# Performance work log

Hardware: AMD Instinct MI355X
Metric: run time of the kernel (lower is better)

Reference implementation:

```python
import jax, jax.numpy as jnp
import numpy as np

OBS_LEN = 16          # observation_len in SnapKV
KERNEL = 5            # AvgPool1d kernel_size
MAX_CACHE_LEN = 2048  # max_cache_length


def _avg_pool1d_nopad(x, k=KERNEL):
    """AvgPool1d(kernel=k, stride=1, padding=k//2, count_include_pad=False) over last axis."""
    S = x.shape[-1]
    pad = k // 2
    zero = jnp.zeros(x.shape[:-1] + (1,), x.dtype)
    c0 = jnp.concatenate([zero, jnp.cumsum(x, axis=-1)], axis=-1)  # [..., S+1]
    i = jnp.arange(S)
    hi = jnp.minimum(i + pad + 1, S)  # exclusive window end
    lo = jnp.maximum(i - pad, 0)      # inclusive window start
    wsum = jnp.take(c0, hi, axis=-1) - jnp.take(c0, lo, axis=-1)
    return wsum / (hi - lo).astype(x.dtype)


def setup_inputs() -> dict:
    key = jax.random.key(0)
    k1, k2, k3 = jax.random.split(key, 3)
    B, H, Q, S, D = 1, 32, 64, 8192, 128
    # realistic attention weights: softmax over key axis
    attn = jax.nn.softmax(jax.random.normal(k1, (B, H, Q, S), jnp.float32), axis=-1)
    k_val = jax.random.normal(k2, (B, H, S, D), jnp.float32)
    v_val = jax.random.normal(k3, (B, H, S, D), jnp.float32)
    input_pos = jnp.arange(S, dtype=jnp.int32)
    return {"attn": attn, "k_val": k_val, "v_val": v_val, "input_pos": input_pos}


def reference(attn, k_val, v_val, input_pos):
    # ---- SnapKV prompt compression (_compress_prompt_w_snapkv) ----
    # priority: mean attention received by each key over the last OBS_LEN queries
    priority = attn[:, :, -OBS_LEN:, :].mean(axis=2)          # [B, H, S]
    attn_history = priority                                    # pre-pooling copy
    pooled = _avg_pool1d_nopad(priority)                       # [B, H, S]
    pooled = pooled.at[:, :, -OBS_LEN:].set(1.0)               # always keep observation window
    _, keep_idxs = jax.lax.top_k(pooled, MAX_CACHE_LEN)        # [B, H, L]
    keep_idxs = jnp.sort(keep_idxs, axis=-1)
    attn_history_c = jnp.take_along_axis(attn_history, keep_idxs, axis=-1)  # [B, H, L]
    idx4 = keep_idxs[..., None]                                # [B, H, L, 1]
    k_compressed = jnp.take_along_axis(k_val, idx4, axis=2)    # [B, H, L, D]
    v_compressed = jnp.take_along_axis(v_val, idx4, axis=2)    # [B, H, L, D]
    # ---- cache fill (update / fill_headwise): compressed tokens fill the whole cache ----
    k_cache = k_compressed
    v_cache = v_compressed
    pos = keep_idxs[0].astype(jnp.int32)                       # head-specific positions, [H, L]
    return k_cache, v_cache, attn_history_c, pos
```

## Files before the change

### kernel.cpp

```cpp
#include <hip/hip_runtime.h>

#define H 32
#define Q 64
#define S 8192
#define D 128
#define OBS 16
#define L 2048

__global__ void k_priority(const float* __restrict__ attn, float* __restrict__ prio) {
    int gid = blockIdx.x;
    int h = gid >> 3;
    int chunk = gid & 7;
    int s4 = chunk * 1024 + threadIdx.x * 4;
    const float4* base = (const float4*)(attn + ((size_t)(h * Q + (Q - OBS)) * S + s4));
    float4 acc = make_float4(0.f, 0.f, 0.f, 0.f);
#pragma unroll
    for (int qq = 0; qq < OBS; ++qq) {
        float4 v = base[qq * (S / 4)];
        acc.x += v.x; acc.y += v.y; acc.z += v.z; acc.w += v.w;
    }
    const float inv = 1.0f / (float)OBS;
    acc.x *= inv; acc.y *= inv; acc.z *= inv; acc.w *= inv;
    *((float4*)(prio + (size_t)h * S + s4)) = acc;
}

__global__ __launch_bounds__(1024) void k_select(const float* __restrict__ prio,
                                                 int* __restrict__ keep,
                                                 float* __restrict__ hist_out,
                                                 float* __restrict__ pos_out) {
    __shared__ float pr[S];
    __shared__ int scan_buf[1024];
    __shared__ unsigned red[16];
    const int h = blockIdx.x;
    const int tid = threadIdx.x;
    const int lane = tid & 63, wid = tid >> 6;

    {
        const float4* src = (const float4*)(prio + (size_t)h * S);
        float4* dst4 = (float4*)pr;
        for (int i = tid; i < S / 4; i += 1024) dst4[i] = src[i];
    }
    __syncthreads();

    unsigned key[8];
    const int s0 = tid * 8;
#pragma unroll
    for (int j = 0; j < 8; ++j) {
        int s = s0 + j;
        float pooled;
        if (s >= S - OBS) {
            pooled = 1.0f;
        } else {
            int lo = s - 2; if (lo < 0) lo = 0;
            int hi = s + 3; if (hi > S) hi = S;
            float sum = 0.f;
            for (int i = lo; i < hi; ++i) sum += pr[i];
            pooled = sum / (float)(hi - lo);
        }
        key[j] = __float_as_uint(pooled);
    }

    unsigned prefix = 0;
    int k = L;
    for (int b = 31; b >= 0; --b) {
        const unsigned bit = 1u << b;
        const unsigned want = prefix | bit;
        const unsigned mask = ~(bit - 1u);
        int cnt = 0;
#pragma unroll
        for (int j = 0; j < 8; ++j) cnt += ((key[j] & mask) == want) ? 1 : 0;
        unsigned c = (unsigned)cnt;
        for (int off = 32; off > 0; off >>= 1) c += __shfl_down(c, off);
        if (lane == 0) red[wid] = c;
        __syncthreads();
        unsigned total = 0;
#pragma unroll
        for (int w = 0; w < 16; ++w) total += red[w];
        __syncthreads();
        if ((int)total >= k) prefix = want; else k -= (int)total;
    }
    const unsigned T = prefix;
    const int needed_eq = k;

    int local_eq = 0;
#pragma unroll
    for (int j = 0; j < 8; ++j) local_eq += (key[j] == T) ? 1 : 0;
    scan_buf[tid] = local_eq;
    __syncthreads();
    for (int off = 1; off < 1024; off <<= 1) {
        int v = scan_buf[tid];
        int add = (tid >= off) ? scan_buf[tid - off] : 0;
        __syncthreads();
        scan_buf[tid] = v + add;
        __syncthreads();
    }
    const int eq_before = scan_buf[tid] - local_eq;

    int sel_mask = 0, sel_count = 0;
    {
        int eqrank = eq_before;
#pragma unroll
        for (int j = 0; j < 8; ++j) {
            bool gt = key[j] > T;
            bool eq = key[j] == T;
            bool sl = gt || (eq && (eqrank < needed_eq));
            if (eq) eqrank++;
            if (sl) { sel_mask |= (1 << j); sel_count++; }
        }
    }
    __syncthreads();

    scan_buf[tid] = sel_count;
    __syncthreads();
    for (int off = 1; off < 1024; off <<= 1) {
        int v = scan_buf[tid];
        int add = (tid >= off) ? scan_buf[tid - off] : 0;
        __syncthreads();
        scan_buf[tid] = v + add;
        __syncthreads();
    }
    int r = scan_buf[tid] - sel_count;

#pragma unroll
    for (int j = 0; j < 8; ++j) {
        if (sel_mask & (1 << j)) {
            int s = s0 + j;
            size_t o = (size_t)h * L + r;
            keep[o] = s;
            pos_out[o] = (float)s;
            hist_out[o] = pr[s];
            r++;
        }
    }
}

__global__ void k_gather(const float* __restrict__ kvK, const float* __restrict__ kvV,
                         const int* __restrict__ keep, float* __restrict__ out) {
    const int tid = threadIdx.x;
    const int row = blockIdx.x * 8 + (tid >> 5);
    const int lane = tid & 31;
    const int tensor = row >> 16;
    const int idx = row & 65535;
    const int h = idx >> 11;
    const int s = keep[idx];
    const float* srcbase = tensor ? kvV : kvK;
    const float4* src = (const float4*)(srcbase + (size_t)(h * S + s) * D);
    float4* dst = (float4*)(out + (size_t)tensor * ((size_t)H * L * D) + (size_t)idx * D);
    dst[lane] = src[lane];
}

extern "C" void kernel_launch(void* const* d_in, const int* in_sizes, int n_in,
                              void* d_out, int out_size, void* d_ws, size_t ws_size,
                              hipStream_t stream) {
    const float* attn = (const float*)d_in[0];
    const float* k_val = (const float*)d_in[1];
    const float* v_val = (const float*)d_in[2];

    float* out = (float*)d_out;
    float* hist = out + (size_t)2 * H * L * D;
    float* pos = hist + (size_t)H * L;

    float* prio = (float*)d_ws;
    int* keep = (int*)((char*)d_ws + (size_t)H * S * sizeof(float));

    k_priority<<<256, 256, 0, stream>>>(attn, prio);
    k_select<<<H, 1024, 0, stream>>>(prio, keep, hist, pos);
    k_gather<<<(2 * H * L) / 8, 256, 0, stream>>>(k_val, v_val, keep, out);
}
```

Measured before the change: 310.0 us.

## Fuse priority reduction into select and replace block scans with wave scans

Folds the observation-window mean into the per-head select kernel, which removes one launch and the priority round-trip through global memory. The pooling window is now loaded into registers once rather than re-read from shared memory, and the radix-select reduction uses shared atomics, cutting one barrier per bit. The two block-wide Hillis-Steele scans become one wave-level shuffle scan on packed greater/equal counts, so ranks are computed directly. The gather handles K and V in the same thread, which halves the block count. The trade-off is that the attention read now runs on only 32 blocks, which may underuse bandwidth compared with the 256-block priority kernel.

```diff
diff --git a/kernel.cpp b/kernel.cpp
--- a/kernel.cpp
+++ b/kernel.cpp
@@ -7,57 +7,63 @@
 #define OBS 16
 #define L 2048
 
-__global__ void k_priority(const float* __restrict__ attn, float* __restrict__ prio) {
-    int gid = blockIdx.x;
-    int h = gid >> 3;
-    int chunk = gid & 7;
-    int s4 = chunk * 1024 + threadIdx.x * 4;
-    const float4* base = (const float4*)(attn + ((size_t)(h * Q + (Q - OBS)) * S + s4));
-    float4 acc = make_float4(0.f, 0.f, 0.f, 0.f);
-#pragma unroll
-    for (int qq = 0; qq < OBS; ++qq) {
-        float4 v = base[qq * (S / 4)];
-        acc.x += v.x; acc.y += v.y; acc.z += v.z; acc.w += v.w;
-    }
-    const float inv = 1.0f / (float)OBS;
-    acc.x *= inv; acc.y *= inv; acc.z *= inv; acc.w *= inv;
-    *((float4*)(prio + (size_t)h * S + s4)) = acc;
-}
-
-__global__ __launch_bounds__(1024) void k_select(const float* __restrict__ prio,
+__global__ __launch_bounds__(1024) void k_select(const float* __restrict__ attn,
                                                  int* __restrict__ keep,
                                                  float* __restrict__ hist_out,
                                                  float* __restrict__ pos_out) {
     __shared__ float pr[S];
-    __shared__ int scan_buf[1024];
-    __shared__ unsigned red[16];
+    __shared__ int wtot[16];
+    __shared__ int rcount[32];
     const int h = blockIdx.x;
     const int tid = threadIdx.x;
     const int lane = tid & 63, wid = tid >> 6;
 
+    if (tid < 32) rcount[tid] = 0;
+
     {
-        const float4* src = (const float4*)(prio + (size_t)h * S);
-        float4* dst4 = (float4*)pr;
-        for (int i = tid; i < S / 4; i += 1024) dst4[i] = src[i];
+        const float* abase = attn + ((size_t)(h * Q + (Q - OBS))) * S;
+        float4 a0 = make_float4(0.f, 0.f, 0.f, 0.f);
+        float4 a1 = make_float4(0.f, 0.f, 0.f, 0.f);
+#pragma unroll
+        for (int q = 0; q < OBS; ++q) {
+            const float4* row = (const float4*)(abase + (size_t)q * S);
+            float4 v0 = row[tid];
+            float4 v1 = row[tid + 1024];
+            a0.x += v0.x; a0.y += v0.y; a0.z += v0.z; a0.w += v0.w;
+            a1.x += v1.x; a1.y += v1.y; a1.z += v1.z; a1.w += v1.w;
+        }
+        const float inv = 1.0f / (float)OBS;
+        a0.x *= inv; a0.y *= inv; a0.z *= inv; a0.w *= inv;
+        a1.x *= inv; a1.y *= inv; a1.z *= inv; a1.w *= inv;
+        ((float4*)pr)[tid] = a0;
+        ((float4*)pr)[tid + 1024] = a1;
     }
     __syncthreads();
 
     unsigned key[8];
     const int s0 = tid * 8;
+    {
+        float w[12];
 #pragma unroll
-    for (int j = 0; j < 8; ++j) {
-        int s = s0 + j;
-        float pooled;
-        if (s >= S - OBS) {
-            pooled = 1.0f;
-        } else {
-            int lo = s - 2; if (lo < 0) lo = 0;
-            int hi = s + 3; if (hi > S) hi = S;
-            float sum = 0.f;
-            for (int i = lo; i < hi; ++i) sum += pr[i];
-            pooled = sum / (float)(hi - lo);
+        for (int i = 0; i < 12; ++i) {
+            int idx = s0 - 2 + i;
+            w[i] = (idx >= 0 && idx < S) ? pr[idx] : 0.f;
         }
-        key[j] = __float_as_uint(pooled);
+#pragma unroll
+        for (int j = 0; j < 8; ++j) {
+            int s = s0 + j;
+            float pooled;
+            if (s >= S - OBS) {
+                pooled = 1.0f;
+            } else {
+                int lo = s - 2; if (lo < 0) lo = 0;
+                int hi = s + 3;
+                float sum = 0.f;
+                for (int i = lo; i < hi; ++i) sum += w[i - s0 + 2];
+                pooled = sum / (float)(hi - lo);
+            }
+            key[j] = __float_as_uint(pooled);
+        }
     }
 
     unsigned prefix = 0;
@@ -69,84 +75,71 @@
         int cnt = 0;
 #pragma unroll
         for (int j = 0; j < 8; ++j) cnt += ((key[j] & mask) == want) ? 1 : 0;
-        unsigned c = (unsigned)cnt;
-        for (int off = 32; off > 0; off >>= 1) c += __shfl_down(c, off);
-        if (lane == 0) red[wid] = c;
+#pragma unroll
+        for (int off = 32; off > 0; off >>= 1) cnt += __shfl_down(cnt, off);
+        if (lane == 0) atomicAdd(&rcount[b], cnt);
         __syncthreads();
-        unsigned total = 0;
-#pragma unroll
-        for (int w = 0; w < 16; ++w) total += red[w];
-        __syncthreads();
-        if ((int)total >= k) prefix = want; else k -= (int)total;
+        int total = rcount[b];
+        if (total >= k) prefix = want; else k -= total;
     }
     const unsigned T = prefix;
     const int needed_eq = k;
 
-    int local_eq = 0;
+    int gt = 0, eq = 0;
 #pragma unroll
-    for (int j = 0; j < 8; ++j) local_eq += (key[j] == T) ? 1 : 0;
-    scan_buf[tid] = local_eq;
+    for (int j = 0; j < 8; ++j) {
+        gt += (key[j] > T) ? 1 : 0;
+        eq += (key[j] == T) ? 1 : 0;
+    }
+    int packed = (gt << 16) | eq;
+    int v = packed;
+#pragma unroll
+    for (int off = 1; off < 64; off <<= 1) {
+        int u = __shfl_up(v, off);
+        if (lane >= off) v += u;
+    }
+    if (lane == 63) wtot[wid] = v;
     __syncthreads();
-    for (int off = 1; off < 1024; off <<= 1) {
-        int v = scan_buf[tid];
-        int add = (tid >= off) ? scan_buf[tid - off] : 0;
-        __syncthreads();
-        scan_buf[tid] = v + add;
-        __syncthreads();
-    }
-    const int eq_before = scan_buf[tid] - local_eq;
+    int base = 0;
+    for (int w = 0; w < wid; ++w) base += wtot[w];
+    int excl = base + v - packed;
+    int gt_before = excl >> 16;
+    int eq_before = excl & 0xffff;
 
-    int sel_mask = 0, sel_count = 0;
     {
-        int eqrank = eq_before;
+        int g = gt_before, e = eq_before;
 #pragma unroll
         for (int j = 0; j < 8; ++j) {
-            bool gt = key[j] > T;
-            bool eq = key[j] == T;
-            bool sl = gt || (eq && (eqrank < needed_eq));
-            if (eq) eqrank++;
-            if (sl) { sel_mask |= (1 << j); sel_count++; }
-        }
-    }
-    __syncthreads();
-
-    scan_buf[tid] = sel_count;
-    __syncthreads();
-    for (int off = 1; off < 1024; off <<= 1) {
-        int v = scan_buf[tid];
-        int add = (tid >= off) ? scan_buf[tid - off] : 0;
-        __syncthreads();
-        scan_buf[tid] = v + add;
-        __syncthreads();
-    }
-    int r = scan_buf[tid] - sel_count;
-
-#pragma unroll
-    for (int j = 0; j < 8; ++j) {
-        if (sel_mask & (1 << j)) {
-            int s = s0 + j;
-            size_t o = (size_t)h * L + r;
-            keep[o] = s;
-            pos_out[o] = (float)s;
-            hist_out[o] = pr[s];
-            r++;
+            bool isgt = key[j] > T;
+            bool iseq = key[j] == T;
+            bool sel = isgt || (iseq && (e < needed_eq));
+            if (sel) {
+                int s = s0 + j;
+                int rank = g + (e < needed_eq ? e : needed_eq);
+                size_t o = (size_t)h * L + rank;
+                keep[o] = s;
+                pos_out[o] = (float)s;
+                hist_out[o] = pr[s];
+            }
+            g += isgt ? 1 : 0;
+            e += iseq ? 1 : 0;
         }
     }
 }
 
-__global__ void k_gather(const float* __restrict__ kvK, const float* __restrict__ kvV,
+__global__ void k_gather(const float* __restrict__ kv_k, const float* __restrict__ kv_v,
                          const int* __restrict__ keep, float* __restrict__ out) {
     const int tid = threadIdx.x;
-    const int row = blockIdx.x * 8 + (tid >> 5);
+    const int idx = blockIdx.x * 8 + (tid >> 5);
     const int lane = tid & 31;
-    const int tensor = row >> 16;
-    const int idx = row & 65535;
     const int h = idx >> 11;
     const int s = keep[idx];
-    const float* srcbase = tensor ? kvV : kvK;
-    const float4* src = (const float4*)(srcbase + (size_t)(h * S + s) * D);
-    float4* dst = (float4*)(out + (size_t)tensor * ((size_t)H * L * D) + (size_t)idx * D);
-    dst[lane] = src[lane];
+    const float4* srcK = (const float4*)(kv_k + (size_t)(h * S + s) * D);
+    const float4* srcV = (const float4*)(kv_v + (size_t)(h * S + s) * D);
+    float4* dstK = (float4*)(out + (size_t)idx * D);
+    float4* dstV = (float4*)(out + ((size_t)H * L + idx) * D);
+    dstK[lane] = srcK[lane];
+    dstV[lane] = srcV[lane];
 }
 
 extern "C" void kernel_launch(void* const* d_in, const int* in_sizes, int n_in,
@@ -160,10 +153,8 @@
     float* hist = out + (size_t)2 * H * L * D;
     float* pos = hist + (size_t)H * L;
 
-    float* prio = (float*)d_ws;
-    int* keep = (int*)((char*)d_ws + (size_t)H * S * sizeof(float));
+    int* keep = (int*)d_ws;
 
-    k_priority<<<256, 256, 0, stream>>>(attn, prio);
-    k_select<<<H, 1024, 0, stream>>>(prio, keep, hist, pos);
-    k_gather<<<(2 * H * L) / 8, 256, 0, stream>>>(k_val, v_val, keep, out);
+    k_select<<<H, 1024, 0, stream>>>(attn, keep, hist, pos);
+    k_gather<<<(H * L) / 8, 256, 0, stream>>>(k_val, v_val, keep, out);
 }
```

Result: no change. 313.4 us (+1.1%).
